# Performance work log

Measured on AMD Instinct MI355X. Metric: run time of the kernel, lower is better.

The kernel has to match this reference:

```python
import jax, jax.numpy as jnp
import numpy as np

NUM_TRACKS = [128, 256, 512, 1024, 2048, 64, 32, 1024]
B, S, D = 8, 2048, 1536
H = len(NUM_TRACKS)
T = max(NUM_TRACKS)  # num_output_tracks (padded)


def setup_inputs() -> dict:
    key = jax.random.key(0)
    kx, kw, kb, ki = jax.random.split(key, 4)
    x = jax.random.normal(kx, (B, S, D), dtype=jnp.float32)
    # Padded per-species weights: columns >= num_tracks[i] are zero, matching the
    # original's jnp.pad of head logits with zeros.
    track_mask = (jnp.arange(T)[None, :] < jnp.asarray(NUM_TRACKS)[:, None]).astype(jnp.float32)  # [H, T]
    W = jax.random.normal(kw, (H, D, T), dtype=jnp.float32) * 0.02
    W = W * track_mask[:, None, :]
    b = jax.random.normal(kb, (H, T), dtype=jnp.float32) * 0.02
    b = b * track_mask
    head_idx = jax.random.randint(ki, (B,), 0, H, dtype=jnp.int32)
    return {"x": x, "head_idx": head_idx, "W": W, "b": b}


def reference(x, head_idx, W, b):
    # Dense compute of ALL species heads (faithful to original which evaluates
    # every head over the full batch), then per-sample selection via head_idx
    # (equivalent to the original's sequential jnp.where masking).
    logits_all = jnp.einsum('bsd,hdt->bhst', x, W) + b[None, :, None, :]  # [B, H, S, T]
    sel = head_idx[:, None, None, None].astype(jnp.int32)                 # [B, 1, 1, 1]
    logits = jnp.take_along_axis(logits_all, sel, axis=1)[:, 0]           # [B, S, T]
    return logits
```

## Files before the change

kernel.cpp:

```cpp
#include <hip/hip_runtime.h>
#include <hip/hip_bf16.h>
#include <stdint.h>

#define NB 8
#define NS 2048
#define ND 1536
#define NT 2048
#define NH 8
#define NK (ND / 32)

__constant__ int c_nlim[NH] = {128, 256, 512, 1024, 2048, 128, 128, 1024};

typedef short bf16x8 __attribute__((ext_vector_type(8)));
typedef unsigned short u16x8 __attribute__((ext_vector_type(8)));
typedef float f32x4 __attribute__((ext_vector_type(4)));

__device__ __forceinline__ unsigned short f2bf(float f) {
    union { float f; unsigned u; } a; a.f = f;
    unsigned r = a.u + 0x7fffu + ((a.u >> 16) & 1u);
    return (unsigned short)(r >> 16);
}

#define XBLK 24576
__global__ void cvt_kernel(const float* __restrict__ x,
                           const float* __restrict__ W,
                           const int* __restrict__ hidx,
                           unsigned short* __restrict__ xb,
                           unsigned short* __restrict__ Wt) {
    const int bid = blockIdx.x;
    const int tid = threadIdx.x;
    if (bid < XBLK) {
        const size_t i = (size_t)bid * 256 + tid;
        float4 v = ((const float4*)x)[i];
        ushort4 o;
        o.x = f2bf(v.x); o.y = f2bf(v.y); o.z = f2bf(v.z); o.w = f2bf(v.w);
        ((ushort4*)xb)[i] = o;
        return;
    }
    const int wid = bid - XBLK;
    const int h = wid / (32 * 24);
    const int rem = wid % (32 * 24);
    const int t0 = (rem % 32) * 64;
    const int d0 = (rem / 32) * 64;
    bool used = false;
    for (int i = 0; i < NB; ++i) used |= (hidx[i] == h);
    if (!used || t0 >= c_nlim[h]) return;

    __shared__ float tile[64][69];
#pragma unroll
    for (int i = 0; i < 4; ++i) {
        const int idx = tid + i * 256;
        const int d = idx >> 4, c = (idx & 15) * 4;
        float4 v = *(const float4*)&W[((size_t)h * ND + d0 + d) * NT + t0 + c];
        tile[d][c] = v.x; tile[d][c + 1] = v.y;
        tile[d][c + 2] = v.z; tile[d][c + 3] = v.w;
    }
    __syncthreads();
    const int t = tid >> 2, dc = (tid & 3) * 16;
    u16x8 o0, o1;
#pragma unroll
    for (int j = 0; j < 8; ++j) o0[j] = f2bf(tile[dc + j][t]);
#pragma unroll
    for (int j = 0; j < 8; ++j) o1[j] = f2bf(tile[dc + 8 + j][t]);
    unsigned short* p = Wt + ((size_t)h * NT + t0 + t) * ND + d0 + dc;
    *(u16x8*)p = o0;
    *(u16x8*)(p + 8) = o1;
}

#define GLDS(g, l)                                                      \
    __builtin_amdgcn_global_load_lds(                                   \
        (const __attribute__((address_space(1))) void*)(g),             \
        (__attribute__((address_space(3))) void*)(l), 16, 0, 0)

__global__ __launch_bounds__(256) void gemm_kernel(
    const unsigned short* __restrict__ xb,
    const unsigned short* __restrict__ wt,
    const float* __restrict__ bias,
    const int* __restrict__ hidx,
    float* __restrict__ out)
{
    const int id = blockIdx.x;
    const int q = id >> 8, r = id & 255;
    const int nr = r & 15;
    const int m0 = (r >> 4) * 128;
    const int n0 = (((nr + 2 * q) & 15)) * 128;
    const int batch = (nr + q) & 7;
    const int h = hidx[batch];
    const int tid = threadIdx.x;
    float* outb = out + (size_t)batch * NS * NT;

    if (n0 >= c_nlim[h]) {
        const int row = tid >> 1;
        const int c0 = (tid & 1) * 64;
        float4 z = make_float4(0.f, 0.f, 0.f, 0.f);
        float4* p = (float4*)(outb + (size_t)(m0 + row) * NT + (n0 + c0));
#pragma unroll
        for (int j = 0; j < 16; ++j) p[j] = z;
        return;
    }

    __shared__ unsigned short As[128 * 32];
    __shared__ unsigned short Bs[128 * 32];

    const int lane = tid & 63;
    const int wave = tid >> 6;
    const int wm = (wave >> 1) * 64;
    const int wn = (wave & 1) * 64;
    const int fr = lane & 15;
    const int fq = (lane >> 4) * 8;

    const int r0 = tid >> 2, kc0 = (tid & 3) * 8;
    const int i1 = tid + 256;
    const int r1 = i1 >> 2, kc1 = (i1 & 3) * 8;

    const unsigned short* ga0 = xb + ((size_t)batch * NS + m0 + r0) * ND + kc0;
    const unsigned short* ga1 = xb + ((size_t)batch * NS + m0 + r1) * ND + kc1;
    const unsigned short* gb0 = wt + ((size_t)h * NT + n0 + r0) * ND + kc0;
    const unsigned short* gb1 = wt + ((size_t)h * NT + n0 + r1) * ND + kc1;
    unsigned short* la0 = As + tid * 8;
    unsigned short* la1 = As + i1 * 8;
    unsigned short* lb0 = Bs + tid * 8;
    unsigned short* lb1 = Bs + i1 * 8;

    f32x4 acc[4][4] = {};

    for (int k0 = 0; k0 < ND; k0 += 32) {
        GLDS(ga0, la0); GLDS(ga1, la1); GLDS(gb0, lb0); GLDS(gb1, lb1);
        __syncthreads();
        bf16x8 af[4], bfr[4];
#pragma unroll
        for (int mi = 0; mi < 4; ++mi)
            af[mi] = *(const bf16x8*)(As + (wm + mi * 16 + fr) * 32 + fq);
#pragma unroll
        for (int ni = 0; ni < 4; ++ni)
            bfr[ni] = *(const bf16x8*)(Bs + (wn + ni * 16 + fr) * 32 + fq);
#pragma unroll
        for (int mi = 0; mi < 4; ++mi)
#pragma unroll
            for (int ni = 0; ni < 4; ++ni)
                acc[mi][ni] = __builtin_amdgcn_mfma_f32_16x16x32_bf16(
                    af[mi], bfr[ni], acc[mi][ni], 0, 0, 0);
        __syncthreads();
        ga0 += 32; ga1 += 32; gb0 += 32; gb1 += 32;
    }

    float bv[4];
#pragma unroll
    for (int ni = 0; ni < 4; ++ni)
        bv[ni] = bias[(size_t)h * NT + n0 + wn + ni * 16 + fr];

    const int rbase = m0 + wm + (lane >> 4) * 4;
#pragma unroll
    for (int mi = 0; mi < 4; ++mi) {
#pragma unroll
        for (int r = 0; r < 4; ++r) {
            float* op = outb + (size_t)(rbase + mi * 16 + r) * NT + n0 + wn + fr;
#pragma unroll
            for (int ni = 0; ni < 4; ++ni)
                op[ni * 16] = acc[mi][ni][r] + bv[ni];
        }
    }
}

extern "C" void kernel_launch(void* const* d_in, const int* in_sizes, int n_in,
                              void* d_out, int out_size, void* d_ws, size_t ws_size,
                              hipStream_t stream) {
    const float* x    = (const float*)d_in[0];
    const int*   hidx = (const int*)d_in[1];
    const float* W    = (const float*)d_in[2];
    const float* bias = (const float*)d_in[3];
    float* out = (float*)d_out;

    unsigned short* xb = (unsigned short*)d_ws;
    unsigned short* wt = xb + (size_t)NB * NS * ND;

    cvt_kernel<<<dim3(XBLK + 32 * 24 * NH), dim3(256), 0, stream>>>(
        x, W, hidx, xb, wt);
    gemm_kernel<<<dim3(2048), dim3(256), 0, stream>>>(xb, wt, bias, hidx, out);
}
```

Measured before the change: 352.9 us.

## Enlarge GEMM tiles, add XOR-swizzled LDS, schedule compute blocks before zero-fill

Each GEMM block now has 512 threads and computes a 256x128 output tile with a K step of 64 instead of 32, which halves the barriers per unit of work and raises A/B reuse. LDS rows are XOR-swizzled per 16-byte chunk to avoid bank conflicts on the fragment reads. Block IDs are remapped so every block that needs a matmul for the active heads launches before the blocks that only write zeros, which should improve load balance. The cost is higher LDS use and register pressure per block, which may lower occupancy.

```diff
diff --git a/kernel.cpp b/kernel.cpp
--- a/kernel.cpp
+++ b/kernel.cpp
@@ -7,9 +7,9 @@
 #define ND 1536
 #define NT 2048
 #define NH 8
-#define NK (ND / 32)
-
-__constant__ int c_nlim[NH] = {128, 256, 512, 1024, 2048, 128, 128, 1024};
+#define NK2 (ND / 64)
+
+__constant__ int c_tiles[NH] = {1, 2, 4, 8, 16, 1, 1, 8};
 
 typedef short bf16x8 __attribute__((ext_vector_type(8)));
 typedef unsigned short u16x8 __attribute__((ext_vector_type(8)));
@@ -44,7 +44,7 @@
     const int d0 = (rem / 32) * 64;
     bool used = false;
     for (int i = 0; i < NB; ++i) used |= (hidx[i] == h);
-    if (!used || t0 >= c_nlim[h]) return;
+    if (!used || t0 >= c_tiles[h] * 128) return;
 
     __shared__ float tile[64][69];
 #pragma unroll
@@ -72,76 +72,116 @@
         (const __attribute__((address_space(1))) void*)(g),             \
         (__attribute__((address_space(3))) void*)(l), 16, 0, 0)
 
-__global__ __launch_bounds__(256) void gemm_kernel(
+__global__ __launch_bounds__(512) void gemm_kernel(
     const unsigned short* __restrict__ xb,
     const unsigned short* __restrict__ wt,
     const float* __restrict__ bias,
     const int* __restrict__ hidx,
     float* __restrict__ out)
 {
+    const int tid = threadIdx.x;
     const int id = blockIdx.x;
-    const int q = id >> 8, r = id & 255;
-    const int nr = r & 15;
-    const int m0 = (r >> 4) * 128;
-    const int n0 = (((nr + 2 * q) & 15)) * 128;
-    const int batch = (nr + q) & 7;
-    const int h = hidx[batch];
-    const int tid = threadIdx.x;
-    float* outb = out + (size_t)batch * NS * NT;
-
-    if (n0 >= c_nlim[h]) {
+
+    int hh[NB], tl[NB];
+    int P = 0;
+#pragma unroll
+    for (int b = 0; b < NB; ++b) {
+        hh[b] = hidx[b];
+        tl[b] = c_tiles[hh[b]];
+        P += tl[b];
+    }
+    const int C = 8 * P;
+
+    int batch, m0, n0;
+    if (id >= C) {
+        const int Pz = 128 - P;
+        const int z = id - C;
+        int p = z % Pz;
+        const int m = z / Pz;
+        int b = 0;
+        while (p >= 16 - tl[b]) { p -= 16 - tl[b]; ++b; }
+        batch = b; n0 = (tl[b] + p) * 128; m0 = m * 256;
+        float* outb = out + (size_t)batch * NS * NT;
         const int row = tid >> 1;
         const int c0 = (tid & 1) * 64;
-        float4 z = make_float4(0.f, 0.f, 0.f, 0.f);
-        float4* p = (float4*)(outb + (size_t)(m0 + row) * NT + (n0 + c0));
-#pragma unroll
-        for (int j = 0; j < 16; ++j) p[j] = z;
+        float4 zv = make_float4(0.f, 0.f, 0.f, 0.f);
+        float4* ptr = (float4*)(outb + (size_t)(m0 + row) * NT + (n0 + c0));
+#pragma unroll
+        for (int j = 0; j < 16; ++j) ptr[j] = zv;
         return;
     }
-
-    __shared__ unsigned short As[128 * 32];
-    __shared__ unsigned short Bs[128 * 32];
+    {
+        int p = id % P;
+        const int m = id / P;
+        int b = 0;
+        while (p >= tl[b]) { p -= tl[b]; ++b; }
+        batch = b; n0 = p * 128; m0 = m * 256;
+    }
+    const int h = hh[batch];
+    float* outb = out + (size_t)batch * NS * NT;
+
+    __shared__ unsigned short As[256 * 64];
+    __shared__ unsigned short Bs[128 * 64];
 
     const int lane = tid & 63;
     const int wave = tid >> 6;
     const int wm = (wave >> 1) * 64;
     const int wn = (wave & 1) * 64;
     const int fr = lane & 15;
-    const int fq = (lane >> 4) * 8;
-
-    const int r0 = tid >> 2, kc0 = (tid & 3) * 8;
-    const int i1 = tid + 256;
-    const int r1 = i1 >> 2, kc1 = (i1 & 3) * 8;
-
-    const unsigned short* ga0 = xb + ((size_t)batch * NS + m0 + r0) * ND + kc0;
-    const unsigned short* ga1 = xb + ((size_t)batch * NS + m0 + r1) * ND + kc1;
-    const unsigned short* gb0 = wt + ((size_t)h * NT + n0 + r0) * ND + kc0;
-    const unsigned short* gb1 = wt + ((size_t)h * NT + n0 + r1) * ND + kc1;
-    unsigned short* la0 = As + tid * 8;
-    unsigned short* la1 = As + i1 * 8;
-    unsigned short* lb0 = Bs + tid * 8;
-    unsigned short* lb1 = Bs + i1 * 8;
+    const int q = lane >> 4;
+
+    const unsigned short* ga[4];
+    unsigned short* la[4];
+#pragma unroll
+    for (int j = 0; j < 4; ++j) {
+        const int c = tid + 512 * j;
+        const int r = c >> 3, gc = (c & 7) ^ (r & 7);
+        ga[j] = xb + ((size_t)batch * NS + m0 + r) * ND + gc * 8;
+        la[j] = As + c * 8;
+    }
+    const unsigned short* gb[2];
+    unsigned short* lb[2];
+#pragma unroll
+    for (int j = 0; j < 2; ++j) {
+        const int c = tid + 512 * j;
+        const int r = c >> 3, gc = (c & 7) ^ (r & 7);
+        gb[j] = wt + ((size_t)h * NT + n0 + r) * ND + gc * 8;
+        lb[j] = Bs + c * 8;
+    }
+
+    const int sw0 = ((q) ^ (fr & 7)) * 8;
+    const int sw1 = ((q + 4) ^ (fr & 7)) * 8;
 
     f32x4 acc[4][4] = {};
 
-    for (int k0 = 0; k0 < ND; k0 += 32) {
-        GLDS(ga0, la0); GLDS(ga1, la1); GLDS(gb0, lb0); GLDS(gb1, lb1);
+    for (int it = 0; it < NK2; ++it) {
+#pragma unroll
+        for (int j = 0; j < 4; ++j) GLDS(ga[j], la[j]);
+#pragma unroll
+        for (int j = 0; j < 2; ++j) GLDS(gb[j], lb[j]);
         __syncthreads();
-        bf16x8 af[4], bfr[4];
-#pragma unroll
-        for (int mi = 0; mi < 4; ++mi)
-            af[mi] = *(const bf16x8*)(As + (wm + mi * 16 + fr) * 32 + fq);
-#pragma unroll
-        for (int ni = 0; ni < 4; ++ni)
-            bfr[ni] = *(const bf16x8*)(Bs + (wn + ni * 16 + fr) * 32 + fq);
-#pragma unroll
-        for (int mi = 0; mi < 4; ++mi)
+#pragma unroll
+        for (int kk = 0; kk < 2; ++kk) {
+            const int sw = kk ? sw1 : sw0;
+            bf16x8 af[4], bfr[4];
+#pragma unroll
+            for (int mi = 0; mi < 4; ++mi)
+                af[mi] = *(const bf16x8*)(As + (wm + mi * 16 + fr) * 64 + sw);
 #pragma unroll
             for (int ni = 0; ni < 4; ++ni)
-                acc[mi][ni] = __builtin_amdgcn_mfma_f32_16x16x32_bf16(
-                    af[mi], bfr[ni], acc[mi][ni], 0, 0, 0);
+                bfr[ni] = *(const bf16x8*)(Bs + (wn + ni * 16 + fr) * 64 + sw);
+#pragma unroll
+            for (int mi = 0; mi < 4; ++mi)
+#pragma unroll
+                for (int ni = 0; ni < 4; ++ni)
+                    acc[mi][ni] = __builtin_amdgcn_mfma_f32_16x16x32_bf16(
+                        af[mi], bfr[ni], acc[mi][ni], 0, 0, 0);
+        }
         __syncthreads();
-        ga0 += 32; ga1 += 32; gb0 += 32; gb1 += 32;
+#pragma unroll
+        for (int j = 0; j < 4; ++j) ga[j] += 64;
+#pragma unroll
+        for (int j = 0; j < 2; ++j) gb[j] += 64;
     }
 
     float bv[4];
@@ -149,7 +189,7 @@
     for (int ni = 0; ni < 4; ++ni)
         bv[ni] = bias[(size_t)h * NT + n0 + wn + ni * 16 + fr];
 
-    const int rbase = m0 + wm + (lane >> 4) * 4;
+    const int rbase = m0 + wm + q * 4;
 #pragma unroll
     for (int mi = 0; mi < 4; ++mi) {
 #pragma unroll
@@ -176,5 +216,5 @@
 
     cvt_kernel<<<dim3(XBLK + 32 * 24 * NH), dim3(256), 0, stream>>>(
         x, W, hidx, xb, wt);
-    gemm_kernel<<<dim3(2048), dim3(256), 0, stream>>>(xb, wt, bias, hidx, out);
-}
+    gemm_kernel<<<dim3(1024), dim3(512), 0, stream>>>(xb, wt, bias, hidx, out);
+}
```

Result: faster. 322.6 us (-8.6%).
